# Performance work log

Measured on AMD Instinct MI355X. Metric: run time of the kernel, lower is better.

## Reference

```python
import jax, jax.numpy as jnp
import numpy as np

HIDDEN = 2048
HEADS = 16
HEAD_DIM = HIDDEN // HEADS


def setup_inputs() -> dict:
    key = jax.random.key(0)
    kx, kq, kk, kv, ko = jax.random.split(key, 5)
    s = 1.0 / np.sqrt(HIDDEN)
    return {
        "x": jax.random.normal(kx, (2, 2048, HIDDEN), dtype=jnp.float32),
        "Wq": jax.random.normal(kq, (HIDDEN, HIDDEN), dtype=jnp.float32) * s,
        "Wk": jax.random.normal(kk, (HIDDEN, HIDDEN), dtype=jnp.float32) * s,
        "Wv": jax.random.normal(kv, (HIDDEN, HIDDEN), dtype=jnp.float32) * s,
        "Wo": jax.random.normal(ko, (HIDDEN, HIDDEN), dtype=jnp.float32) * s,
    }


def reference(x, Wq, Wk, Wv, Wo):
    B, S, H = x.shape
    nh, hd = HEADS, HEAD_DIM
    # projections (nn.Linear: y = x @ W.T; here W stored as [in, out] so x @ W)
    q = (x @ Wq).reshape(B, S, nh, hd).transpose(0, 2, 1, 3)  # [B,nh,S,hd]
    k = (x @ Wk).reshape(B, S, nh, hd).transpose(0, 2, 1, 3)
    v = (x @ Wv).reshape(B, S, nh, hd).transpose(0, 2, 1, 3)
    scores = jnp.einsum("bhqd,bhkd->bhqk", q, k) / jnp.sqrt(jnp.float32(hd))
    causal = jnp.tril(jnp.ones((S, S), dtype=bool))  # keep lower triangle
    scores = jnp.where(causal, scores, jnp.finfo(scores.dtype).min)
    attn = jax.nn.softmax(scores, axis=-1)
    out = jnp.einsum("bhqk,bhkd->bhqd", attn, v)
    out = out.transpose(0, 2, 1, 3).reshape(B, S, H)
    return out @ Wo
```

## Files before the change

### kernel.cpp

```cpp
#include <hip/hip_runtime.h>
#include <stdint.h>

typedef unsigned short u16;
typedef __bf16 bf16x8 __attribute__((ext_vector_type(8)));
typedef short s4 __attribute__((ext_vector_type(4)));
typedef float f32x4 __attribute__((ext_vector_type(4)));

#define B_ 2
#define S_ 2048
#define H_ 2048
#define NH_ 16
#define HD_ 128

#define SL2f (0.08838834764831845f * 1.4426950408889634f)

__device__ __forceinline__ u16 f2bf(float f) {
    uint32_t u = __float_as_uint(f);
    u += 0x7fff + ((u >> 16) & 1);
    return (u16)(u >> 16);
}

__device__ __forceinline__ uint32_t pk_bf16(float lo, float hi) {
    return __builtin_amdgcn_perm(__float_as_uint(hi), __float_as_uint(lo), 0x07060302u);
}

__device__ __forceinline__ void gl_lds16(const u16* g, u16* l) {
    __builtin_amdgcn_global_load_lds(
        (const __attribute__((address_space(1))) void*)g,
        (__attribute__((address_space(3))) void*)l, 16, 0, 0);
}

union U2S4 { uint2 u; s4 s; };

__global__ __launch_bounds__(256) void prep_kernel(
        const float* __restrict__ x,
        const float* __restrict__ w0, const float* __restrict__ w1,
        const float* __restrict__ w2, const float* __restrict__ w3,
        u16* __restrict__ xb, u16* __restrict__ dqkv, u16* __restrict__ dwo) {
    int z = blockIdx.z;
    int tx = threadIdx.x, ty = threadIdx.y;
    if (z == 4) {
        int tid = ty * 32 + tx;
        size_t base = ((size_t)(blockIdx.y * 64 + blockIdx.x)) * 2048 + tid * 8;
#pragma unroll
        for (int i = 0; i < 2; i++) {
            float4 v = *(const float4*)&x[base + i * 4];
            ushort4 o;
            o.x = f2bf(v.x); o.y = f2bf(v.y); o.z = f2bf(v.z); o.w = f2bf(v.w);
            *(ushort4*)&xb[base + i * 4] = o;
        }
        return;
    }
    const float* src = (z == 0) ? w0 : (z == 1) ? w1 : (z == 2) ? w2 : w3;
    u16* dst = (z < 3) ? (dqkv + (size_t)z * H_ * H_) : dwo;
    __shared__ float tile[32][33];
    int n0 = blockIdx.x * 32, k0 = blockIdx.y * 32;
#pragma unroll
    for (int i = 0; i < 4; i++)
        tile[ty + i * 8][tx] = src[(size_t)(k0 + ty + i * 8) * H_ + n0 + tx];
    __syncthreads();
#pragma unroll
    for (int i = 0; i < 4; i++)
        dst[(size_t)(n0 + ty + i * 8) * H_ + k0 + tx] = f2bf(tile[tx][ty + i * 8]);
}

template <int MODE>
__global__ __launch_bounds__(256, 2) void gemm_bt(
        const u16* __restrict__ A, const u16* __restrict__ Bt, float* __restrict__ Cout,
        u16* __restrict__ q, u16* __restrict__ k, u16* __restrict__ v,
        int M, int N, int K) {
    __shared__ u16 sm[2 * 128 * 64];
    u16* As = sm;
    u16* Bs = sm + 128 * 64;
    int tid = threadIdx.x;
    int w = tid >> 6, lane = tid & 63, quad = lane >> 4, l16 = lane & 15;
    int wm = w >> 1, wn = w & 1;
    int m0 = blockIdx.y * 128, n0 = blockIdx.x * 128;

    f32x4 acc[4][4];
#pragma unroll
    for (int mi = 0; mi < 4; mi++)
#pragma unroll
        for (int ni = 0; ni < 4; ni++)
            acc[mi][ni] = (f32x4){0.f, 0.f, 0.f, 0.f};

    for (int k0 = 0; k0 < K; k0 += 64) {
        const u16* ga = A + (size_t)m0 * K + k0;
        const u16* gb = Bt + (size_t)n0 * K + k0;
#pragma unroll
        for (int j = 0; j < 4; j++) {
            int base = (j * 4 + w) * 64;
            int p = base + lane;
            int row = p >> 3;
            int c = (p & 7) ^ (row & 7);
            gl_lds16(&ga[(size_t)row * K + c * 8], &As[base * 8]);
            gl_lds16(&gb[(size_t)row * K + c * 8], &Bs[base * 8]);
        }
        __syncthreads();
#pragma unroll
        for (int ks = 0; ks < 2; ks++) {
            bf16x8 af[4], bf[4];
#pragma unroll
            for (int mi = 0; mi < 4; mi++) {
                int row = wm * 64 + mi * 16 + l16;
                af[mi] = *(const bf16x8*)&As[row * 64 + (((ks * 4 + quad) ^ (row & 7)) * 8)];
            }
#pragma unroll
            for (int ni = 0; ni < 4; ni++) {
                int row = wn * 64 + ni * 16 + l16;
                bf[ni] = *(const bf16x8*)&Bs[row * 64 + (((ks * 4 + quad) ^ (row & 7)) * 8)];
            }
#pragma unroll
            for (int mi = 0; mi < 4; mi++)
#pragma unroll
                for (int ni = 0; ni < 4; ni++)
                    acc[mi][ni] = __builtin_amdgcn_mfma_f32_16x16x32_bf16(af[mi], bf[ni], acc[mi][ni], 0, 0, 0);
        }
        __syncthreads();
    }

    if (MODE == 0 && n0 >= 4096) {
#pragma unroll
        for (int mi = 0; mi < 4; mi++) {
#pragma unroll
            for (int ni = 0; ni < 4; ni++) {
                int nl = wn * 64 + ni * 16 + l16;
#pragma unroll
                for (int r = 0; r < 4; r++) {
                    int ml = wm * 64 + mi * 16 + quad * 4 + r;
                    sm[nl * 128 + (((ml >> 3) ^ (nl & 15)) * 8) + (ml & 7)] = f2bf(acc[mi][ni][r]);
                }
            }
        }
        __syncthreads();
        int b = m0 >> 11, s0 = m0 & 2047;
#pragma unroll
        for (int i = 0; i < 8; i++) {
            int cu = tid + i * 256;
            int nl = cu >> 4, mc = cu & 15;
            int4 val = *(const int4*)&sm[nl * 128 + ((mc ^ (nl & 15)) * 8)];
            int ngl = (n0 - 4096) + nl;
            int h = ngl >> 7, d = ngl & 127;
            *(int4*)&v[((size_t)((b * NH_ + h) * HD_ + d)) * S_ + s0 + mc * 8] = val;
        }
    } else {
#pragma unroll
        for (int mi = 0; mi < 4; mi++) {
#pragma unroll
            for (int ni = 0; ni < 4; ni++) {
                int ng = n0 + wn * 64 + ni * 16 + l16;
#pragma unroll
                for (int r = 0; r < 4; r++) {
                    int mg = m0 + wm * 64 + mi * 16 + quad * 4 + r;
                    float val = acc[mi][ni][r];
                    if (MODE == 0) {
                        int which = ng >> 11;
                        int rem = ng & 2047;
                        int h = rem >> 7, d = rem & 127;
                        int b = mg >> 11, s = mg & 2047;
                        if (which == 0)
                            q[((size_t)((b * NH_ + h) * S_ + s)) * HD_ + d] = f2bf(val * SL2f);
                        else
                            k[((size_t)((b * NH_ + h) * S_ + s)) * HD_ + d] = f2bf(val);
                    } else {
                        Cout[(size_t)mg * N + ng] = val;
                    }
                }
            }
        }
    }
}

__global__ __launch_bounds__(256, 2) void flash_kernel(
        const u16* __restrict__ Q, const u16* __restrict__ Kb,
        const u16* __restrict__ VT, u16* __restrict__ Ctx) {
    __shared__ u16 Ks[2][64 * 128];
    __shared__ u16 Vs[2][128 * 64];
    int tid = threadIdx.x;
    int w = tid >> 6, lane = tid & 63, quad = lane >> 4, l16 = lane & 15;

    int id = blockIdx.x;
    int bh = id & 31;
    int b = bh >> 4, h = bh & 15;
    int pair = id >> 5;
    int qts = pair, qtl = 31 - pair;
    int n0 = qts + 1;

    size_t bhoff = ((size_t)b * NH_ + h) * S_ * HD_;
    const u16* Qp = Q + bhoff;
    const u16* Kp = Kb + bhoff;
    const u16* Vp = VT + bhoff;

    auto stageK = [&](int t, int buf) {
        int kv0 = ((t >= n0) ? (t - n0) : t) * 64;
#pragma unroll
        for (int j = 0; j < 4; j++) {
            int base = (j * 4 + w) * 64;
            int p = base + lane;
            int row = p >> 4;
            int c = (p & 15) ^ (row & 15);
            gl_lds16(&Kp[(size_t)(kv0 + row) * HD_ + c * 8], &Ks[buf][base * 8]);
        }
    };
    auto stageV = [&](int t, int buf) {
        int kv0 = ((t >= n0) ? (t - n0) : t) * 64;
#pragma unroll
        for (int j = 0; j < 4; j++) {
            int base = (j * 4 + w) * 64;
            int p = base + lane;
            int row = p >> 3;
            int c = (p & 7) ^ (row & 7);
            gl_lds16(&Vp[(size_t)row * S_ + kv0 + c * 8], &Vs[buf][base * 8]);
        }
    };

    int q0 = qts * 64;
    int qg = q0 + w * 16 + l16;
    bf16x8 qf[4];
#pragma unroll
    for (int ks = 0; ks < 4; ks++)
        qf[ks] = *(const bf16x8*)&Qp[(size_t)qg * HD_ + ks * 32 + quad * 8];

    float l_part = 0.f;
    f32x4 ao[8];
#pragma unroll
    for (int dt = 0; dt < 8; dt++) ao[dt] = (f32x4){0.f, 0.f, 0.f, 0.f};

    auto epilogue = [&]() {
        float l = l_part;
        l += __shfl_xor(l, 16);
        l += __shfl_xor(l, 32);
        float inv = 1.0f / l;
        size_t base = ((size_t)b * S_ + qg) * H_ + h * HD_;
#pragma unroll
        for (int dt = 0; dt < 8; dt++) {
            u16 o0 = f2bf(ao[dt][0] * inv), o1 = f2bf(ao[dt][1] * inv);
            u16 o2 = f2bf(ao[dt][2] * inv), o3 = f2bf(ao[dt][3] * inv);
            uint2 st;
            st.x = (uint32_t)o0 | ((uint32_t)o1 << 16);
            st.y = (uint32_t)o2 | ((uint32_t)o3 << 16);
            *(uint2*)&Ctx[base + dt * 16 + quad * 4] = st;
        }
    };

    stageK(0, 0);
    stageV(0, 0);

    for (int t = 0; t < 33; t++) {
        if (t == n0) {
            epilogue();
            q0 = qtl * 64;
            qg = q0 + w * 16 + l16;
#pragma unroll
            for (int ks = 0; ks < 4; ks++)
                qf[ks] = *(const bf16x8*)&Qp[(size_t)qg * HD_ + ks * 32 + quad * 8];
            l_part = 0.f;
#pragma unroll
            for (int dt = 0; dt < 8; dt++) ao[dt] = (f32x4){0.f, 0.f, 0.f, 0.f};
        }
        int buf = t & 1;
        __syncthreads();

        f32x4 sc[4];
#pragma unroll
        for (int nt = 0; nt < 4; nt++) {
            sc[nt] = (f32x4){0.f, 0.f, 0.f, 0.f};
            int row = nt * 16 + l16;
#pragma unroll
            for (int ks = 0; ks < 4; ks++) {
                bf16x8 kf = *(const bf16x8*)&Ks[buf][row * 128 + (((ks * 4 + quad) ^ (row & 15)) * 8)];
                sc[nt] = __builtin_amdgcn_mfma_f32_16x16x32_bf16(kf, qf[ks], sc[nt], 0, 0, 0);
            }
        }

        __syncthreads();

        if (t + 1 < 33) {
            stageK(t + 1, buf ^ 1);
            stageV(t + 1, buf ^ 1);
        }

        bool diag = (t == n0 - 1) || (t == 32);
        U2S4 pk[4];
        if (!diag) {
#pragma unroll
            for (int nt = 0; nt < 4; nt++) {
                float p0 = exp2f(sc[nt][0]), p1 = exp2f(sc[nt][1]);
                float p2 = exp2f(sc[nt][2]), p3 = exp2f(sc[nt][3]);
                l_part += (p0 + p1) + (p2 + p3);
                pk[nt].u.x = pk_bf16(p0, p1);
                pk[nt].u.y = pk_bf16(p2, p3);
            }
        } else {
            int kvb = q0 + quad * 4;
#pragma unroll
            for (int nt = 0; nt < 4; nt++) {
                int kv = kvb + nt * 16;
                float p0 = (kv + 0 > qg) ? 0.f : exp2f(sc[nt][0]);
                float p1 = (kv + 1 > qg) ? 0.f : exp2f(sc[nt][1]);
                float p2 = (kv + 2 > qg) ? 0.f : exp2f(sc[nt][2]);
                float p3 = (kv + 3 > qg) ? 0.f : exp2f(sc[nt][3]);
                l_part += (p0 + p1) + (p2 + p3);
                pk[nt].u.x = pk_bf16(p0, p1);
                pk[nt].u.y = pk_bf16(p2, p3);
            }
        }

#pragma unroll
        for (int kt = 0; kt < 4; kt++) {
#pragma unroll
            for (int dt = 0; dt < 8; dt++) {
                int d = dt * 16 + l16;
                int c = kt * 2 + (quad >> 1);
                s4 va = *(const s4*)&Vs[buf][d * 64 + ((c ^ (d & 7)) * 8) + (quad & 1) * 4];
                ao[dt] = __builtin_amdgcn_mfma_f32_16x16x16bf16_1k(va, pk[kt].s, ao[dt], 0, 0, 0);
            }
        }
    }
    epilogue();
}

extern "C" void kernel_launch(void* const* d_in, const int* in_sizes, int n_in,
                              void* d_out, int out_size, void* d_ws, size_t ws_size,
                              hipStream_t stream) {
    const float* x  = (const float*)d_in[0];
    const float* Wq = (const float*)d_in[1];
    const float* Wk = (const float*)d_in[2];
    const float* Wv = (const float*)d_in[3];
    const float* Wo = (const float*)d_in[4];
    float* out = (float*)d_out;

    const size_t MB = 1024 * 1024;
    char* ws = (char*)d_ws;
    u16* Xb    = (u16*)(ws);
    u16* WqkvT = (u16*)(ws + 16 * MB);
    u16* WoT   = (u16*)(ws + 40 * MB);
    u16* Qb    = (u16*)(ws + 48 * MB);
    u16* Kbuf  = (u16*)(ws + 64 * MB);
    u16* VT    = (u16*)(ws + 80 * MB);
    u16* Ctx   = (u16*)(ws + 96 * MB);

    prep_kernel<<<dim3(64, 64, 5), dim3(32, 8), 0, stream>>>(x, Wq, Wk, Wv, Wo, Xb, WqkvT, WoT);
    gemm_bt<0><<<dim3(48, 32), 256, 0, stream>>>(Xb, WqkvT, nullptr, Qb, Kbuf, VT, 4096, 6144, 2048);
    flash_kernel<<<512, 256, 0, stream>>>(Qb, Kbuf, VT, Ctx);
    gemm_bt<1><<<dim3(16, 32), 256, 0, stream>>>(Ctx, WoT, out, nullptr, nullptr, nullptr, 4096, 2048, 2048);
}
```

Measured before the change: 349.0 us.

## Widen GEMM tiles to 128x256 with multi-buffered async LDS prefetch

Both GEMMs now run 512-thread blocks on 128x256 output tiles. The A tile is double-buffered and the B tile triple-buffered in LDS, with loads for the next one or two k-steps issued ahead of the MFMA work on the current step. A manual vmcnt wait plus a single barrier replaces the two __syncthreads per iteration. The goal is to hide global-to-LDS latency and get more reuse per loaded tile, at the cost of 128KB of LDS per block, which limits occupancy to one block per CU.

```diff
diff --git a/kernel.cpp b/kernel.cpp
--- a/kernel.cpp
+++ b/kernel.cpp
@@ -65,17 +65,16 @@
 }
 
 template <int MODE>
-__global__ __launch_bounds__(256, 2) void gemm_bt(
+__global__ __launch_bounds__(512, 2) void gemm_bt(
         const u16* __restrict__ A, const u16* __restrict__ Bt, float* __restrict__ Cout,
         u16* __restrict__ q, u16* __restrict__ k, u16* __restrict__ v,
         int M, int N, int K) {
-    __shared__ u16 sm[2 * 128 * 64];
-    u16* As = sm;
-    u16* Bs = sm + 128 * 64;
+    __shared__ u16 sm[65536];
     int tid = threadIdx.x;
     int w = tid >> 6, lane = tid & 63, quad = lane >> 4, l16 = lane & 15;
-    int wm = w >> 1, wn = w & 1;
-    int m0 = blockIdx.y * 128, n0 = blockIdx.x * 128;
+    int wm = w >> 2, wn = w & 3;
+    int m0 = blockIdx.y * 128, n0 = blockIdx.x * 256;
+    const int NT = K >> 6;
 
     f32x4 acc[4][4];
 #pragma unroll
@@ -84,22 +83,48 @@
         for (int ni = 0; ni < 4; ni++)
             acc[mi][ni] = (f32x4){0.f, 0.f, 0.f, 0.f};
 
-    for (int k0 = 0; k0 < K; k0 += 64) {
-        const u16* ga = A + (size_t)m0 * K + k0;
-        const u16* gb = Bt + (size_t)n0 * K + k0;
+    auto stageA = [&](int kt) {
+        const u16* ga = A + (size_t)m0 * K + kt * 64;
+        u16* As = sm + (kt & 1) * 8192;
+#pragma unroll
+        for (int j = 0; j < 2; j++) {
+            int p = j * 512 + tid;
+            int row = p >> 3, c = (p & 7) ^ (row & 7);
+            gl_lds16(&ga[(size_t)row * K + c * 8], &As[(j * 512 + w * 64) * 8]);
+        }
+    };
+    auto stageB = [&](int kt) {
+        const u16* gb = Bt + (size_t)n0 * K + kt * 64;
+        u16* Bs = sm + 16384 + (kt % 3) * 16384;
 #pragma unroll
         for (int j = 0; j < 4; j++) {
-            int base = (j * 4 + w) * 64;
-            int p = base + lane;
-            int row = p >> 3;
-            int c = (p & 7) ^ (row & 7);
-            gl_lds16(&ga[(size_t)row * K + c * 8], &As[base * 8]);
-            gl_lds16(&gb[(size_t)row * K + c * 8], &Bs[base * 8]);
-        }
-        __syncthreads();
+            int p = j * 512 + tid;
+            int row = p >> 3, c = (p & 7) ^ (row & 7);
+            gl_lds16(&gb[(size_t)row * K + c * 8], &Bs[(j * 512 + w * 64) * 8]);
+        }
+    };
+
+    stageA(0);
+    stageB(0);
+    stageB(1);
+
+    for (int kt = 0; kt < NT; kt++) {
+        __builtin_amdgcn_sched_barrier(0);
+        if (kt == NT - 1)
+            asm volatile("s_waitcnt vmcnt(0) lgkmcnt(0)" ::: "memory");
+        else
+            asm volatile("s_waitcnt vmcnt(4) lgkmcnt(0)" ::: "memory");
+        __builtin_amdgcn_s_barrier();
+        __builtin_amdgcn_sched_barrier(0);
+
+        if (kt + 1 < NT) stageA(kt + 1);
+        if (kt + 2 < NT) stageB(kt + 2);
+
+        const u16* As = sm + (kt & 1) * 8192;
+        const u16* Bs = sm + 16384 + (kt % 3) * 16384;
 #pragma unroll
         for (int ks = 0; ks < 2; ks++) {
-            bf16x8 af[4], bf[4];
+            bf16x8 af[4], bfr[4];
 #pragma unroll
             for (int mi = 0; mi < 4; mi++) {
                 int row = wm * 64 + mi * 16 + l16;
@@ -108,18 +133,18 @@
 #pragma unroll
             for (int ni = 0; ni < 4; ni++) {
                 int row = wn * 64 + ni * 16 + l16;
-                bf[ni] = *(const bf16x8*)&Bs[row * 64 + (((ks * 4 + quad) ^ (row & 7)) * 8)];
+                bfr[ni] = *(const bf16x8*)&Bs[row * 64 + (((ks * 4 + quad) ^ (row & 7)) * 8)];
             }
 #pragma unroll
             for (int mi = 0; mi < 4; mi++)
 #pragma unroll
                 for (int ni = 0; ni < 4; ni++)
-                    acc[mi][ni] = __builtin_amdgcn_mfma_f32_16x16x32_bf16(af[mi], bf[ni], acc[mi][ni], 0, 0, 0);
-        }
+                    acc[mi][ni] = __builtin_amdgcn_mfma_f32_16x16x32_bf16(af[mi], bfr[ni], acc[mi][ni], 0, 0, 0);
+        }
+    }
+
+    if (MODE == 0 && n0 >= 4096) {
         __syncthreads();
-    }
-
-    if (MODE == 0 && n0 >= 4096) {
 #pragma unroll
         for (int mi = 0; mi < 4; mi++) {
 #pragma unroll
@@ -136,7 +161,7 @@
         int b = m0 >> 11, s0 = m0 & 2047;
 #pragma unroll
         for (int i = 0; i < 8; i++) {
-            int cu = tid + i * 256;
+            int cu = tid + i * 512;
             int nl = cu >> 4, mc = cu & 15;
             int4 val = *(const int4*)&sm[nl * 128 + ((mc ^ (nl & 15)) * 8)];
             int ngl = (n0 - 4096) + nl;
@@ -341,7 +366,7 @@
     u16* Ctx   = (u16*)(ws + 96 * MB);
 
     prep_kernel<<<dim3(64, 64, 5), dim3(32, 8), 0, stream>>>(x, Wq, Wk, Wv, Wo, Xb, WqkvT, WoT);
-    gemm_bt<0><<<dim3(48, 32), 256, 0, stream>>>(Xb, WqkvT, nullptr, Qb, Kbuf, VT, 4096, 6144, 2048);
+    gemm_bt<0><<<dim3(24, 32), 512, 0, stream>>>(Xb, WqkvT, nullptr, Qb, Kbuf, VT, 4096, 6144, 2048);
     flash_kernel<<<512, 256, 0, stream>>>(Qb, Kbuf, VT, Ctx);
-    gemm_bt<1><<<dim3(16, 32), 256, 0, stream>>>(Ctx, WoT, out, nullptr, nullptr, nullptr, 4096, 2048, 2048);
-}
+    gemm_bt<1><<<dim3(8, 32), 512, 0, stream>>>(Ctx, WoT, out, nullptr, nullptr, nullptr, 4096, 2048, 2048);
+}
```

New measurement: 352.6 us. No clear change (+1.0%).
